# Kernel tuning notes

Hardware: AMD Instinct MI355X
Metric: run time of the kernel (lower is better)

Reference implementation:

```python
import jax, jax.numpy as jnp
import numpy as np

N_NODES = 50000
N_EDGES = 150000
N_TRIS = 100000
F = 256
L = 4


def setup_inputs() -> dict:
    key = jax.random.key(0)
    ks = jax.random.split(key, 8)
    x = jax.random.normal(ks[0], (N_EDGES, F), dtype=jnp.float32)
    edge_nodes = jax.random.randint(ks[1], (N_EDGES, 2), 0, N_NODES)
    tri_edges = jax.random.randint(ks[2], (N_TRIS, 3), 0, N_EDGES)
    tri_signs = (jax.random.randint(ks[3], (N_TRIS, 3), 0, 2) * 2 - 1).astype(jnp.int32)
    std = float(np.sqrt(2.0 / (F + F)))  # xavier_uniform-equivalent std
    W0_stack = jax.random.normal(ks[4], (L, F, F), dtype=jnp.float32) * std
    W1_stack = jax.random.normal(ks[5], (L, F, F), dtype=jnp.float32) * std
    W2_stack = jax.random.normal(ks[6], (L, F, F), dtype=jnp.float32) * std
    W0_L = jax.random.normal(ks[7], (F, 1), dtype=jnp.float32) * float(np.sqrt(2.0 / (F + 1)))
    return {"x": x, "W0_stack": W0_stack, "W1_stack": W1_stack, "W2_stack": W2_stack,
            "W0_L": W0_L, "edge_nodes": edge_nodes, "tri_edges": tri_edges, "tri_signs": tri_signs}


def _b1_mm(edge_nodes, y):
    # B1 @ y : [E,F] -> [N,F];  B1[u,e] = -1, B1[v,e] = +1
    u, v = edge_nodes[:, 0], edge_nodes[:, 1]
    out = jnp.zeros((N_NODES, y.shape[1]), y.dtype)
    return out.at[u].add(-y).at[v].add(y)


def _b1t_mm(edge_nodes, z):
    # B1.T @ z : [N,F] -> [E,F]
    return z[edge_nodes[:, 1]] - z[edge_nodes[:, 0]]


def _b2t_mm(tri_edges, signs, y):
    # B2.T @ y : [E,F] -> [T,F]
    return jnp.einsum('tkf,tk->tf', y[tri_edges], signs)


def _b2_mm(tri_edges, signs, w):
    # B2 @ w : [T,F] -> [E,F]
    contrib = w[:, None, :] * signs[:, :, None]  # [T,3,F]
    out = jnp.zeros((N_EDGES, w.shape[1]), w.dtype)
    return out.at[tri_edges.reshape(-1)].add(contrib.reshape(-1, w.shape[1]))


def reference(x, W0_stack, W1_stack, W2_stack, W0_L, edge_nodes, tri_edges, tri_signs):
    signs = tri_signs.astype(x.dtype)
    for i in range(L):
        d2 = _b2_mm(tri_edges, signs, _b2t_mm(tri_edges, signs, x @ W2_stack[i]))
        d1 = x @ W1_stack[i]
        d0 = _b1t_mm(edge_nodes, _b1_mm(edge_nodes, x @ W0_stack[i]))
        x = jax.nn.relu(d2 + d1 + d0)
    return _b1_mm(edge_nodes, x @ W0_L)  # [N_NODES, 1]
```

## Files before the change

### kernel.cpp

```cpp
#include <hip/hip_runtime.h>

#define M_EDGES 150000
#define NN_NODES 50000
#define N_TRIS  100000
#define F 256
#define NLAYERS 4

#define T0 1172
#define T1 391
#define T2 782
#define TZW (T1 + T2)
#define GR_PAD 1176
#define TPX8 147

typedef __attribute__((ext_vector_type(8))) __bf16 bf16x8;
typedef __attribute__((ext_vector_type(4))) float f32x4;

__device__ inline unsigned short f2bf(float f) {
    unsigned int u = __float_as_uint(f);
    u += 0x7fff + ((u >> 16) & 1);
    return (unsigned short)(u >> 16);
}
__device__ inline float bf2f(unsigned short h) {
    return __uint_as_float(((unsigned int)h) << 16);
}

__device__ inline void async16(const void* g, void* l) {
    __builtin_amdgcn_global_load_lds(
        (const __attribute__((address_space(1))) void*)g,
        (__attribute__((address_space(3))) void*)l, 16, 0, 0);
}


#define GEMM_KLOOP(Asrc, wsel, nrows)                                       \
    for (int k0 = 0; k0 < 256; k0 += 32) {                                  \
        {                                                                   \
            int row = tid >> 2;                                             \
            int g   = (tid & 3) ^ ((row >> 1) & 3);                         \
            int gr  = bm0 + row;                                            \
            if (gr > (nrows) - 1) gr = (nrows) - 1;                         \
            async16((Asrc) + (size_t)gr * 256 + k0 + g * 8,                 \
                    As + (size_t)wbase * 8);                                \
        }                                                                   \
        _Pragma("unroll")                                                   \
        for (int ss = 0; ss < 2; ss++) {                                    \
            int i   = ss * 512 + tid;                                       \
            int row = i >> 2;                                               \
            int g   = (i & 3) ^ ((row >> 1) & 3);                           \
            async16((wsel) + (size_t)row * 256 + k0 + g * 8,                \
                    Bs + (size_t)(ss * 512 + wbase) * 8);                   \
        }                                                                   \
        asm volatile("s_waitcnt vmcnt(0)" ::: "memory");                    \
        __syncthreads();                                                    \
        bf16x8 a[4], bfr[4];                                                \
        _Pragma("unroll")                                                   \
        for (int i = 0; i < 4; i++) {                                       \
            int rr = wm * 64 + i * 16 + lm;                                 \
            a[i] = *(const bf16x8*)(As + rr * 32 +                          \
                                    ((lh ^ ((rr >> 1) & 3)) * 8));          \
        }                                                                   \
        _Pragma("unroll")                                                   \
        for (int j = 0; j < 4; j++) {                                       \
            int rr = wn * 64 + j * 16 + lm;                                 \
            bfr[j] = *(const bf16x8*)(Bs + rr * 32 +                        \
                                      ((lh ^ ((rr >> 1) & 3)) * 8));        \
        }                                                                   \
        _Pragma("unroll")                                                   \
        for (int i = 0; i < 4; i++)                                         \
            _Pragma("unroll")                                               \
            for (int j = 0; j < 4; j++)                                     \
                cacc[i][j] = __builtin_amdgcn_mfma_f32_16x16x32_bf16(       \
                    bfr[j], a[i], cacc[i][j], 0, 0, 0);                     \
        __syncthreads();                                                    \
    }

__global__ __launch_bounds__(512) void gemm_zw(
    const unsigned short* __restrict__ sb,
    const unsigned short* __restrict__ qb,
    const unsigned short* __restrict__ wt,
    unsigned short* __restrict__ zb,
    unsigned short* __restrict__ wb)
{
    __shared__ unsigned short As[128 * 32];
    __shared__ unsigned short Bs[256 * 32];

    const int b    = blockIdx.x;
    const int tile = (b & 7) * TPX8 + (b >> 3);
    if (tile >= TZW) return;

    int seg, tloc;
    if (tile < T1) { seg = 1; tloc = tile; }
    else           { seg = 2; tloc = tile - T1; }
    const unsigned short* Asrc = (seg == 1) ? sb : qb;
    const int nrows = (seg == 1) ? NN_NODES : N_TRIS;
    const unsigned short* wsel = wt + seg * 65536;
    unsigned short* dst = (seg == 1) ? zb : wb;

    const int tid  = threadIdx.x;
    const int bm0  = tloc * 128;
    const int wid  = tid >> 6;
    const int lane = tid & 63;
    const int lm   = lane & 15;
    const int lh   = lane >> 4;
    const int wm   = wid >> 2;
    const int wn   = wid & 3;
    const int wbase = tid & ~63;

    f32x4 cacc[4][4];
#pragma unroll
    for (int i = 0; i < 4; i++)
#pragma unroll
        for (int j = 0; j < 4; j++) cacc[i][j] = (f32x4){0.f, 0.f, 0.f, 0.f};

    GEMM_KLOOP(Asrc, wsel, nrows)

#pragma unroll
    for (int i = 0; i < 4; i++) {
        int grow = bm0 + wm * 64 + i * 16 + lm;
        if (grow < nrows) {
#pragma unroll
            for (int j = 0; j < 4; j++) {
                int col = wn * 64 + j * 16 + lh * 4;
                ushort4 r;
                r.x = f2bf(cacc[i][j][0]);
                r.y = f2bf(cacc[i][j][1]);
                r.z = f2bf(cacc[i][j][2]);
                r.w = f2bf(cacc[i][j][3]);
                *(ushort4*)(dst + (size_t)grow * 256 + col) = r;
            }
        }
    }
}

__global__ __launch_bounds__(512) void gemm_y1_relu(
    unsigned short* __restrict__ xb,
    const unsigned short* __restrict__ wt,
    const unsigned short* __restrict__ wb,
    const unsigned short* __restrict__ zb,
    const int* __restrict__ en,
    const int* __restrict__ eoff,
    const int* __restrict__ eadj,
    const float* __restrict__ wl,
    float* __restrict__ p,
    int last)
{
    __shared__ __align__(16) unsigned short smem[128 * 256];
    unsigned short* const As = smem;
    unsigned short* const Bs = smem + 128 * 32;

    const int b    = blockIdx.x;
    const int tile = (b & 7) * TPX8 + (b >> 3);
    if (tile >= T0) return;

    const int tid  = threadIdx.x;
    const int bm0  = tile * 128;
    const int wid  = tid >> 6;
    const int lane = tid & 63;
    const int lm   = lane & 15;
    const int lh   = lane >> 4;
    const int wm   = wid >> 2;
    const int wn   = wid & 3;
    const int wbase = tid & ~63;

    f32x4 cacc[4][4];
#pragma unroll
    for (int i = 0; i < 4; i++)
#pragma unroll
        for (int j = 0; j < 4; j++) cacc[i][j] = (f32x4){0.f, 0.f, 0.f, 0.f};

    GEMM_KLOOP(xb, wt, M_EDGES)

#pragma unroll
    for (int i = 0; i < 4; i++) {
        int lr  = wm * 64 + i * 16 + lm;
        int key = (lr & 7) << 4;
#pragma unroll
        for (int j = 0; j < 4; j++) {
            int colb = wn * 128 + j * 32 + lh * 8;
            ushort4 r;
            r.x = f2bf(cacc[i][j][0]);
            r.y = f2bf(cacc[i][j][1]);
            r.z = f2bf(cacc[i][j][2]);
            r.w = f2bf(cacc[i][j][3]);
            *(ushort4*)((char*)smem + (size_t)lr * 512 + (colb ^ key)) = r;
        }
    }
    __syncthreads();

    const int f = lane * 4;
    for (int r8 = 0; r8 < 16; r8++) {
        int lr = r8 * 8 + wid;
        int e  = bm0 + lr;
        if (e >= M_EDGES) break;
        ushort4 yv = *(const ushort4*)((const char*)smem + (size_t)lr * 512 +
                                       ((lane * 8) ^ ((lr & 7) << 4)));
        int u = en[2 * e], v = en[2 * e + 1];
        ushort4 zv4 = *(const ushort4*)(zb + (size_t)v * 256 + f);
        ushort4 zu4 = *(const ushort4*)(zb + (size_t)u * 256 + f);
        float sx = bf2f(yv.x) + bf2f(zv4.x) - bf2f(zu4.x);
        float sy = bf2f(yv.y) + bf2f(zv4.y) - bf2f(zu4.y);
        float sz = bf2f(yv.z) + bf2f(zv4.z) - bf2f(zu4.z);
        float sw = bf2f(yv.w) + bf2f(zv4.w) - bf2f(zu4.w);
        int beg = eoff[e], end = eoff[e + 1];
        int i2 = beg;
        for (; i2 + 1 < end; i2 += 2) {
            int ta = eadj[i2], tb = eadj[i2 + 1];
            float sa  = (ta & 1) ? -1.f : 1.f;
            float sgb = (tb & 1) ? -1.f : 1.f;
            ushort4 wa  = *(const ushort4*)(wb + (size_t)(ta >> 1) * 256 + f);
            ushort4 wbv = *(const ushort4*)(wb + (size_t)(tb >> 1) * 256 + f);
            sx += sa * bf2f(wa.x) + sgb * bf2f(wbv.x);
            sy += sa * bf2f(wa.y) + sgb * bf2f(wbv.y);
            sz += sa * bf2f(wa.z) + sgb * bf2f(wbv.z);
            sw += sa * bf2f(wa.w) + sgb * bf2f(wbv.w);
        }
        if (i2 < end) {
            int ta = eadj[i2];
            float sa = (ta & 1) ? -1.f : 1.f;
            ushort4 wa = *(const ushort4*)(wb + (size_t)(ta >> 1) * 256 + f);
            sx += sa * bf2f(wa.x);
            sy += sa * bf2f(wa.y);
            sz += sa * bf2f(wa.z);
            sw += sa * bf2f(wa.w);
        }
        sx = fmaxf(sx, 0.f);
        sy = fmaxf(sy, 0.f);
        sz = fmaxf(sz, 0.f);
        sw = fmaxf(sw, 0.f);
        if (!last) {
            ushort4 r;
            r.x = f2bf(sx); r.y = f2bf(sy); r.z = f2bf(sz); r.w = f2bf(sw);
            *(ushort4*)(xb + (size_t)e * 256 + f) = r;
        } else {
            float4 wv = *(const float4*)(wl + f);
            float s = sx * wv.x + sy * wv.y + sz * wv.z + sw * wv.w;
#pragma unroll
            for (int off = 32; off > 0; off >>= 1)
                s += __shfl_down(s, off, 64);
            if (lane == 0) p[e] = s;
        }
    }
}

__global__ __launch_bounds__(256) void count_nodes(
    const int* __restrict__ en, int* __restrict__ cnt)
{
    int e = blockIdx.x * 256 + threadIdx.x;
    if (e < M_EDGES) {
        atomicAdd(&cnt[en[2 * e]], 1);
        atomicAdd(&cnt[en[2 * e + 1]], 1);
    }
}

__global__ __launch_bounds__(256) void count_tris(
    const int* __restrict__ te, int* __restrict__ cnt)
{
    int t = blockIdx.x * 256 + threadIdx.x;
    if (t < N_TRIS) {
#pragma unroll
        for (int k = 0; k < 3; k++) atomicAdd(&cnt[te[3 * t + k]], 1);
    }
}

__global__ __launch_bounds__(256) void scan_block(
    const int* __restrict__ cnt, int* __restrict__ off,
    int* __restrict__ partial, int n)
{
    __shared__ int s[256];
    int t = threadIdx.x;
    int gid = blockIdx.x * 256 + t;
    int v = (gid < n) ? cnt[gid] : 0;
    s[t] = v;
    __syncthreads();
    for (int o = 1; o < 256; o <<= 1) {
        int x = (t >= o) ? s[t - o] : 0;
        __syncthreads();
        s[t] += x;
        __syncthreads();
    }
    if (gid < n) off[gid] = s[t] - v;
    if (t == 255) partial[blockIdx.x] = s[255];
}

__global__ __launch_bounds__(1024) void scan_partial(int* __restrict__ partial, int nb)
{
    __shared__ int s[1024];
    int t = threadIdx.x;
    int v = (t < nb) ? partial[t] : 0;
    s[t] = v;
    __syncthreads();
    for (int o = 1; o < 1024; o <<= 1) {
        int x = (t >= o) ? s[t - o] : 0;
        __syncthreads();
        s[t] += x;
        __syncthreads();
    }
    if (t < nb) partial[t] = s[t] - v;
}

__global__ __launch_bounds__(256) void scan_add(
    int* __restrict__ off, int* __restrict__ cursor,
    const int* __restrict__ partial, int n, int total)
{
    int gid = blockIdx.x * 256 + threadIdx.x;
    if (gid == 0) off[n] = total;
    if (gid < n) {
        int o = off[gid] + partial[blockIdx.x];
        off[gid] = o;
        cursor[gid] = o;
    }
}

__global__ __launch_bounds__(256) void fill_nodes(
    const int* __restrict__ en, int* __restrict__ cursor, int* __restrict__ adj)
{
    int e = blockIdx.x * 256 + threadIdx.x;
    if (e < M_EDGES) {
        int u = en[2 * e], v = en[2 * e + 1];
        adj[atomicAdd(&cursor[u], 1)] = (e << 1);
        adj[atomicAdd(&cursor[v], 1)] = (e << 1) | 1;
    }
}

__global__ __launch_bounds__(256) void fill_tris(
    const int* __restrict__ te, const int* __restrict__ ts,
    int* __restrict__ cursor, int* __restrict__ adj)
{
    int t = blockIdx.x * 256 + threadIdx.x;
    if (t < N_TRIS) {
#pragma unroll
        for (int k = 0; k < 3; k++) {
            int e = te[3 * t + k];
            int neg = (ts[3 * t + k] < 0) ? 1 : 0;
            adj[atomicAdd(&cursor[e], 1)] = (t << 1) | neg;
        }
    }
}

#define ZN_BLOCKS (NN_NODES / 4)
#define WT_BLOCKS (N_TRIS / 4)

__global__ __launch_bounds__(256) void agg_fused(
    const unsigned short* __restrict__ xb,
    const int* __restrict__ noff,
    const int* __restrict__ nadj,
    unsigned short* __restrict__ sbuf,
    const int* __restrict__ te,
    const int* __restrict__ ts,
    unsigned short* __restrict__ qbuf)
{
    int lane = threadIdx.x & 63;
    int f = lane * 4;
    if (blockIdx.x < ZN_BLOCKS) {
        int n = blockIdx.x * 4 + (threadIdx.x >> 6);
        int beg = noff[n], end = noff[n + 1];
        float ax = 0.f, ay = 0.f, az = 0.f, aw = 0.f;
        int i = beg;
        for (; i + 1 < end; i += 2) {
            int ea = nadj[i], eb = nadj[i + 1];
            float sa = (ea & 1) ? 1.f : -1.f;
            float sgb = (eb & 1) ? 1.f : -1.f;
            ushort4 va = *(const ushort4*)(xb + (size_t)(ea >> 1) * 256 + f);
            ushort4 vb = *(const ushort4*)(xb + (size_t)(eb >> 1) * 256 + f);
            ax += sa * bf2f(va.x) + sgb * bf2f(vb.x);
            ay += sa * bf2f(va.y) + sgb * bf2f(vb.y);
            az += sa * bf2f(va.z) + sgb * bf2f(vb.z);
            aw += sa * bf2f(va.w) + sgb * bf2f(vb.w);
        }
        if (i < end) {
            int ea = nadj[i];
            float sa = (ea & 1) ? 1.f : -1.f;
            ushort4 va = *(const ushort4*)(xb + (size_t)(ea >> 1) * 256 + f);
            ax += sa * bf2f(va.x);
            ay += sa * bf2f(va.y);
            az += sa * bf2f(va.z);
            aw += sa * bf2f(va.w);
        }
        ushort4 r;
        r.x = f2bf(ax); r.y = f2bf(ay); r.z = f2bf(az); r.w = f2bf(aw);
        *(ushort4*)(sbuf + (size_t)n * 256 + f) = r;
    } else {
        int t = (blockIdx.x - ZN_BLOCKS) * 4 + (threadIdx.x >> 6);
        int e0 = te[3 * t + 0], e1 = te[3 * t + 1], e2 = te[3 * t + 2];
        float s0 = (float)ts[3 * t + 0];
        float s1 = (float)ts[3 * t + 1];
        float s2 = (float)ts[3 * t + 2];
        ushort4 a4 = *(const ushort4*)(xb + (size_t)e0 * 256 + f);
        ushort4 b4 = *(const ushort4*)(xb + (size_t)e1 * 256 + f);
        ushort4 d4 = *(const ushort4*)(xb + (size_t)e2 * 256 + f);
        ushort4 r;
        r.x = f2bf(s0 * bf2f(a4.x) + s1 * bf2f(b4.x) + s2 * bf2f(d4.x));
        r.y = f2bf(s0 * bf2f(a4.y) + s1 * bf2f(b4.y) + s2 * bf2f(d4.y));
        r.z = f2bf(s0 * bf2f(a4.z) + s1 * bf2f(b4.z) + s2 * bf2f(d4.z));
        r.w = f2bf(s0 * bf2f(a4.w) + s1 * bf2f(b4.w) + s2 * bf2f(d4.w));
        *(ushort4*)(qbuf + (size_t)t * 256 + f) = r;
    }
}

__global__ __launch_bounds__(256) void out_nodes(
    const float* __restrict__ p,
    const int* __restrict__ noff,
    const int* __restrict__ nadj,
    float* __restrict__ out)
{
    int n = blockIdx.x * 256 + threadIdx.x;
    if (n >= NN_NODES) return;
    int beg = noff[n], end = noff[n + 1];
    float s = 0.f;
    for (int i = beg; i < end; i++) {
        int ent = nadj[i];
        float sg = (ent & 1) ? 1.f : -1.f;
        s += sg * p[ent >> 1];
    }
    out[n] = s;
}

__global__ __launch_bounds__(256) void cvt_x(
    const float* __restrict__ x, unsigned short* __restrict__ xb)
{
    int idx = blockIdx.x * 256 + threadIdx.x;
    float4 v = *(const float4*)(x + (size_t)idx * 4);
    ushort4 r;
    r.x = f2bf(v.x); r.y = f2bf(v.y); r.z = f2bf(v.z); r.w = f2bf(v.w);
    *(ushort4*)(xb + (size_t)idx * 4) = r;
}

__global__ __launch_bounds__(256) void cvt_w(
    const float* __restrict__ W0, const float* __restrict__ W1,
    const float* __restrict__ W2, unsigned short* __restrict__ wt)
{
    int idx = blockIdx.x * 256 + threadIdx.x;
    int l = idx / (3 * 65536);
    int rem = idx - l * (3 * 65536);
    int seg = rem >> 16;
    int n = (rem >> 8) & 255;
    int k = rem & 255;
    const float* src = (seg == 0) ? W1 : (seg == 1) ? W0 : W2;
    wt[idx] = f2bf(src[(size_t)l * 65536 + k * 256 + n]);
}

extern "C" void kernel_launch(void* const* d_in, const int* in_sizes, int n_in,
                              void* d_out, int out_size, void* d_ws, size_t ws_size,
                              hipStream_t stream)
{
    const float* x0  = (const float*)d_in[0];
    const float* W0s = (const float*)d_in[1];
    const float* W1s = (const float*)d_in[2];
    const float* W2s = (const float*)d_in[3];
    const float* WL  = (const float*)d_in[4];
    const int*   en  = (const int*)d_in[5];
    const int*   te  = (const int*)d_in[6];
    const int*   ts  = (const int*)d_in[7];
    float* out = (float*)d_out;

    const size_t MF = (size_t)M_EDGES * F;
    unsigned short* xb = (unsigned short*)d_ws;
    unsigned short* y1 = xb + MF;
    unsigned short* sbuf = y1 + MF;
    unsigned short* qbuf = sbuf + (size_t)NN_NODES * 256;
    unsigned short* wt = qbuf + (size_t)N_TRIS * 256;
    unsigned short* wb = wt + (size_t)4 * 3 * 65536;
    unsigned short* zb = wb + (size_t)N_TRIS * 256;
    float* p = (float*)(zb + (size_t)NN_NODES * 256);
    int* noff = (int*)(p + M_EDGES);
    int* ncur = noff + (NN_NODES + 1);
    int* nadj = ncur + NN_NODES;
    int* eoff = nadj + 2 * M_EDGES;
    int* ecur = eoff + (M_EDGES + 1);
    int* eadj = ecur + M_EDGES;
    int* part = eadj + 3 * N_TRIS;

    cvt_w<<<(4 * 3 * 65536) / 256, 256, 0, stream>>>(W0s, W1s, W2s, wt);
    cvt_x<<<(int)(MF / 4 / 256), 256, 0, stream>>>(x0, xb);

    const int nbN = (NN_NODES + 255) / 256;
    const int nbE = (M_EDGES + 255) / 256;
    hipMemsetAsync(ncur, 0, NN_NODES * sizeof(int), stream);
    hipMemsetAsync(ecur, 0, M_EDGES * sizeof(int), stream);
    count_nodes<<<nbE, 256, 0, stream>>>(en, ncur);
    count_tris<<<(N_TRIS + 255) / 256, 256, 0, stream>>>(te, ecur);
    scan_block<<<nbN, 256, 0, stream>>>(ncur, noff, part, NN_NODES);
    scan_partial<<<1, 1024, 0, stream>>>(part, nbN);
    scan_add<<<nbN, 256, 0, stream>>>(noff, ncur, part, NN_NODES, 2 * M_EDGES);
    fill_nodes<<<nbE, 256, 0, stream>>>(en, ncur, nadj);
    scan_block<<<nbE, 256, 0, stream>>>(ecur, eoff, part, M_EDGES);
    scan_partial<<<1, 1024, 0, stream>>>(part, nbE);
    scan_add<<<nbE, 256, 0, stream>>>(eoff, ecur, part, M_EDGES, 3 * N_TRIS);
    fill_tris<<<(N_TRIS + 255) / 256, 256, 0, stream>>>(te, ts, ecur, eadj);

    for (int l = 0; l < NLAYERS; l++) {
        agg_fused<<<ZN_BLOCKS + WT_BLOCKS, 256, 0, stream>>>(
            xb, noff, nadj, sbuf, te, ts, qbuf);
        gemm_zw<<<GR_PAD, 512, 0, stream>>>(
            sbuf, qbuf, wt + (size_t)l * 3 * 65536, zb, wb);
        gemm_y1_relu<<<GR_PAD, 512, 0, stream>>>(
            xb, wt + (size_t)l * 3 * 65536, wb, zb, en, eoff, eadj,
            WL, p, (l == NLAYERS - 1) ? 1 : 0);
    }

    out_nodes<<<(NN_NODES + 255) / 256, 256, 0, stream>>>(p, noff, nadj, out);
}
```

Measured before the change: 1.205 ms.

## Halve epilogue LDS staging in GEMM kernel and shuffle-broadcast node adjacency

The fused GEMM+ReLU kernel now stages its output tile through shared memory in two 64-row halves instead of one 128-row tile. This cuts the LDS allocation to 32KB, which can raise occupancy, at the cost of an extra barrier pair per half. The node-aggregation kernel now loads up to 64 adjacency entries with a single coalesced wavefront load and broadcasts them with __shfl, replacing the serial per-entry scalar loads. Nodes with degree above 64 fall back to the original loop.

```diff
diff --git a/kernel.cpp b/kernel.cpp
--- a/kernel.cpp
+++ b/kernel.cpp
@@ -144,7 +144,7 @@
     float* __restrict__ p,
     int last)
 {
-    __shared__ __align__(16) unsigned short smem[128 * 256];
+    __shared__ __align__(16) unsigned short smem[64 * 256];
     unsigned short* const As = smem;
     unsigned short* const Bs = smem + 128 * 32;
 
@@ -170,74 +170,80 @@
 
     GEMM_KLOOP(xb, wt, M_EDGES)
 
-#pragma unroll
-    for (int i = 0; i < 4; i++) {
-        int lr  = wm * 64 + i * 16 + lm;
-        int key = (lr & 7) << 4;
-#pragma unroll
-        for (int j = 0; j < 4; j++) {
-            int colb = wn * 128 + j * 32 + lh * 8;
-            ushort4 r;
-            r.x = f2bf(cacc[i][j][0]);
-            r.y = f2bf(cacc[i][j][1]);
-            r.z = f2bf(cacc[i][j][2]);
-            r.w = f2bf(cacc[i][j][3]);
-            *(ushort4*)((char*)smem + (size_t)lr * 512 + (colb ^ key)) = r;
-        }
-    }
-    __syncthreads();
-
     const int f = lane * 4;
-    for (int r8 = 0; r8 < 16; r8++) {
-        int lr = r8 * 8 + wid;
-        int e  = bm0 + lr;
-        if (e >= M_EDGES) break;
-        ushort4 yv = *(const ushort4*)((const char*)smem + (size_t)lr * 512 +
-                                       ((lane * 8) ^ ((lr & 7) << 4)));
-        int u = en[2 * e], v = en[2 * e + 1];
-        ushort4 zv4 = *(const ushort4*)(zb + (size_t)v * 256 + f);
-        ushort4 zu4 = *(const ushort4*)(zb + (size_t)u * 256 + f);
-        float sx = bf2f(yv.x) + bf2f(zv4.x) - bf2f(zu4.x);
-        float sy = bf2f(yv.y) + bf2f(zv4.y) - bf2f(zu4.y);
-        float sz = bf2f(yv.z) + bf2f(zv4.z) - bf2f(zu4.z);
-        float sw = bf2f(yv.w) + bf2f(zv4.w) - bf2f(zu4.w);
-        int beg = eoff[e], end = eoff[e + 1];
-        int i2 = beg;
-        for (; i2 + 1 < end; i2 += 2) {
-            int ta = eadj[i2], tb = eadj[i2 + 1];
-            float sa  = (ta & 1) ? -1.f : 1.f;
-            float sgb = (tb & 1) ? -1.f : 1.f;
-            ushort4 wa  = *(const ushort4*)(wb + (size_t)(ta >> 1) * 256 + f);
-            ushort4 wbv = *(const ushort4*)(wb + (size_t)(tb >> 1) * 256 + f);
-            sx += sa * bf2f(wa.x) + sgb * bf2f(wbv.x);
-            sy += sa * bf2f(wa.y) + sgb * bf2f(wbv.y);
-            sz += sa * bf2f(wa.z) + sgb * bf2f(wbv.z);
-            sw += sa * bf2f(wa.w) + sgb * bf2f(wbv.w);
-        }
-        if (i2 < end) {
-            int ta = eadj[i2];
-            float sa = (ta & 1) ? -1.f : 1.f;
-            ushort4 wa = *(const ushort4*)(wb + (size_t)(ta >> 1) * 256 + f);
-            sx += sa * bf2f(wa.x);
-            sy += sa * bf2f(wa.y);
-            sz += sa * bf2f(wa.z);
-            sw += sa * bf2f(wa.w);
-        }
-        sx = fmaxf(sx, 0.f);
-        sy = fmaxf(sy, 0.f);
-        sz = fmaxf(sz, 0.f);
-        sw = fmaxf(sw, 0.f);
-        if (!last) {
-            ushort4 r;
-            r.x = f2bf(sx); r.y = f2bf(sy); r.z = f2bf(sz); r.w = f2bf(sw);
-            *(ushort4*)(xb + (size_t)e * 256 + f) = r;
-        } else {
-            float4 wv = *(const float4*)(wl + f);
-            float s = sx * wv.x + sy * wv.y + sz * wv.z + sw * wv.w;
-#pragma unroll
-            for (int off = 32; off > 0; off >>= 1)
-                s += __shfl_down(s, off, 64);
-            if (lane == 0) p[e] = s;
+    for (int h = 0; h < 2; h++) {
+        __syncthreads();
+        if (wm == h) {
+#pragma unroll
+            for (int i = 0; i < 4; i++) {
+                int lrow = i * 16 + lm;
+                int key  = (lrow & 7) << 4;
+#pragma unroll
+                for (int j = 0; j < 4; j++) {
+                    int colb = wn * 128 + j * 32 + lh * 8;
+                    ushort4 r;
+                    r.x = f2bf(cacc[i][j][0]);
+                    r.y = f2bf(cacc[i][j][1]);
+                    r.z = f2bf(cacc[i][j][2]);
+                    r.w = f2bf(cacc[i][j][3]);
+                    *(ushort4*)((char*)smem + (size_t)lrow * 512 +
+                                (colb ^ key)) = r;
+                }
+            }
+        }
+        __syncthreads();
+
+        for (int r8 = 0; r8 < 8; r8++) {
+            int lr = r8 * 8 + wid;
+            int e  = bm0 + h * 64 + lr;
+            if (e >= M_EDGES) break;
+            ushort4 yv = *(const ushort4*)((const char*)smem +
+                          (size_t)lr * 512 + ((lane * 8) ^ ((lr & 7) << 4)));
+            int u = en[2 * e], v = en[2 * e + 1];
+            ushort4 zv4 = *(const ushort4*)(zb + (size_t)v * 256 + f);
+            ushort4 zu4 = *(const ushort4*)(zb + (size_t)u * 256 + f);
+            float sx = bf2f(yv.x) + bf2f(zv4.x) - bf2f(zu4.x);
+            float sy = bf2f(yv.y) + bf2f(zv4.y) - bf2f(zu4.y);
+            float sz = bf2f(yv.z) + bf2f(zv4.z) - bf2f(zu4.z);
+            float sw = bf2f(yv.w) + bf2f(zv4.w) - bf2f(zu4.w);
+            int beg = eoff[e], end = eoff[e + 1];
+            int i2 = beg;
+            for (; i2 + 1 < end; i2 += 2) {
+                int ta = eadj[i2], tb = eadj[i2 + 1];
+                float sa  = (ta & 1) ? -1.f : 1.f;
+                float sgb = (tb & 1) ? -1.f : 1.f;
+                ushort4 wa  = *(const ushort4*)(wb + (size_t)(ta >> 1) * 256 + f);
+                ushort4 wbv = *(const ushort4*)(wb + (size_t)(tb >> 1) * 256 + f);
+                sx += sa * bf2f(wa.x) + sgb * bf2f(wbv.x);
+                sy += sa * bf2f(wa.y) + sgb * bf2f(wbv.y);
+                sz += sa * bf2f(wa.z) + sgb * bf2f(wbv.z);
+                sw += sa * bf2f(wa.w) + sgb * bf2f(wbv.w);
+            }
+            if (i2 < end) {
+                int ta = eadj[i2];
+                float sa = (ta & 1) ? -1.f : 1.f;
+                ushort4 wa = *(const ushort4*)(wb + (size_t)(ta >> 1) * 256 + f);
+                sx += sa * bf2f(wa.x);
+                sy += sa * bf2f(wa.y);
+                sz += sa * bf2f(wa.z);
+                sw += sa * bf2f(wa.w);
+            }
+            sx = fmaxf(sx, 0.f);
+            sy = fmaxf(sy, 0.f);
+            sz = fmaxf(sz, 0.f);
+            sw = fmaxf(sw, 0.f);
+            if (!last) {
+                ushort4 r;
+                r.x = f2bf(sx); r.y = f2bf(sy); r.z = f2bf(sz); r.w = f2bf(sw);
+                *(ushort4*)(xb + (size_t)e * 256 + f) = r;
+            } else {
+                float4 wv = *(const float4*)(wl + f);
+                float s = sx * wv.x + sy * wv.y + sz * wv.z + sw * wv.w;
+#pragma unroll
+                for (int off = 32; off > 0; off >>= 1)
+                    s += __shfl_down(s, off, 64);
+                if (lane == 0) p[e] = s;
+            }
         }
     }
 }
@@ -354,10 +360,16 @@
     if (blockIdx.x < ZN_BLOCKS) {
         int n = blockIdx.x * 4 + (threadIdx.x >> 6);
         int beg = noff[n], end = noff[n + 1];
+        int deg = end - beg;
+        int cl = beg + lane;
+        if (cl > 2 * M_EDGES - 1) cl = 2 * M_EDGES - 1;
+        int entL = nadj[cl];
+        int dmax = (deg < 64) ? deg : 64;
         float ax = 0.f, ay = 0.f, az = 0.f, aw = 0.f;
-        int i = beg;
-        for (; i + 1 < end; i += 2) {
-            int ea = nadj[i], eb = nadj[i + 1];
+        int j = 0;
+        for (; j + 1 < dmax; j += 2) {
+            int ea = __shfl(entL, j, 64);
+            int eb = __shfl(entL, j + 1, 64);
             float sa = (ea & 1) ? 1.f : -1.f;
             float sgb = (eb & 1) ? 1.f : -1.f;
             ushort4 va = *(const ushort4*)(xb + (size_t)(ea >> 1) * 256 + f);
@@ -367,7 +379,16 @@
             az += sa * bf2f(va.z) + sgb * bf2f(vb.z);
             aw += sa * bf2f(va.w) + sgb * bf2f(vb.w);
         }
-        if (i < end) {
+        if (j < dmax) {
+            int ea = __shfl(entL, j, 64);
+            float sa = (ea & 1) ? 1.f : -1.f;
+            ushort4 va = *(const ushort4*)(xb + (size_t)(ea >> 1) * 256 + f);
+            ax += sa * bf2f(va.x);
+            ay += sa * bf2f(va.y);
+            az += sa * bf2f(va.z);
+            aw += sa * bf2f(va.w);
+        }
+        for (int i = beg + 64; i < end; i++) {
             int ea = nadj[i];
             float sa = (ea & 1) ? 1.f : -1.f;
             ushort4 va = *(const ushort4*)(xb + (size_t)(ea >> 1) * 256 + f);
```

After: 1.453 ms. 20.5% more time.
